# Kernel optimization log

Hardware: AMD Instinct MI355X
Metric: run time of the kernel (lower is better)

Reference implementation:

```python
import jax, jax.numpy as jnp
import numpy as np

N_NODES = 100000
N_EDGES = 1600000
IN_FEATS = 128
OUT_FEATS = 64


def setup_inputs() -> dict:
    key = jax.random.key(0)
    k1, k2, k3, k4 = jax.random.split(key, 4)
    feat = jax.random.normal(k1, (N_NODES, IN_FEATS), dtype=jnp.float32)
    W = jax.random.normal(k2, (IN_FEATS, OUT_FEATS), dtype=jnp.float32) * (1.0 / np.sqrt(IN_FEATS))
    src = jax.random.randint(k3, (N_EDGES,), 0, N_NODES, dtype=jnp.int64)
    dst = jax.random.randint(k4, (N_EDGES,), 0, N_NODES, dtype=jnp.int64)
    return {"feat": feat, "W": W, "src": src, "dst": dst}


def reference(feat, W, src, dst):
    # Linear projection (bias=False): homogeneous graph -> shared fc
    ft = feat @ W  # [N, out]

    # per-edge dot-product score: e_ij = <ft[src], ft[dst]>
    a = jnp.sum(ft[src] * ft[dst], axis=-1)  # [E]

    # edge softmax segmented by destination node (numerically stable)
    neg_inf = jnp.finfo(a.dtype).min
    m = jax.ops.segment_max(a, dst, num_segments=N_NODES)  # [N]
    m = jnp.where(m == neg_inf, 0.0, m)  # guard zero-in-degree nodes
    e = jnp.exp(a - m[dst])  # [E]
    s = jax.ops.segment_sum(e, dst, num_segments=N_NODES)  # [N]
    s = jnp.where(s == 0.0, 1.0, s)
    sa = e / s[dst]  # [E]

    # weighted scatter-sum aggregation: out[i] = sum_{j in N(i)} sa_ij * ft[j]
    rst = jax.ops.segment_sum(ft[src] * sa[:, None], dst, num_segments=N_NODES)
    return rst
```

## Files before the change

### kernel.cpp

```cpp
#include <hip/hip_runtime.h>
#include <hip/hip_fp16.h>
#include <math.h>

#define N_NODES 100000
#define N_EDGES 1600000
#define IN_F    128
#define OUT_F   64
#define K_BKT     196
#define BKT_SHIFT 9
#define BKT_NODES 512
#define BKT_CAP   10240
#define QCAP      3072
#define CHUNK     4096
#define PBLKS     ((N_EDGES + CHUNK - 1) / CHUNK)
#define LTILES    (N_NODES / 16)
#define LBLKS     ((LTILES + 3) / 4)

typedef _Float16 half8 __attribute__((ext_vector_type(8)));
typedef _Float16 h2 __attribute__((ext_vector_type(2)));
typedef _Float16 h4 __attribute__((ext_vector_type(4)));
typedef __fp16   q2v __attribute__((ext_vector_type(2)));
typedef float    f32x4 __attribute__((ext_vector_type(4)));

__device__ __forceinline__ float fdot2f(h2 a, h2 b, float c) {
#if __has_builtin(__builtin_amdgcn_fdot2)
    return __builtin_amdgcn_fdot2(__builtin_bit_cast(q2v, a), __builtin_bit_cast(q2v, b), c, false);
#else
    return (float)a[0] * (float)b[0] + (float)a[1] * (float)b[1] + c;
#endif
}

#if __has_builtin(__builtin_amdgcn_update_dpp)
#define DPP_ADD(x, ctrl)                                                                  \
    (x) += __builtin_bit_cast(float, __builtin_amdgcn_update_dpp(                         \
               0, __builtin_bit_cast(int, (x)), (ctrl), 0xF, 0xF, true))
#define REDUCE16(x) do { DPP_ADD(x, 0xB1); DPP_ADD(x, 0x4E); \
                         DPP_ADD(x, 0x141); DPP_ADD(x, 0x140); } while (0)
#else
#define REDUCE16(x) do { x += __shfl_xor(x, 1); x += __shfl_xor(x, 2); \
                         x += __shfl_xor(x, 4); x += __shfl_xor(x, 8); } while (0)
#endif


__global__ __launch_bounds__(256) void partition_linear_kernel(const int* __restrict__ src,
                                                               const int* __restrict__ dst,
                                                               unsigned* __restrict__ staging,
                                                               int* __restrict__ pcnt,
                                                               int* __restrict__ pbase,
                                                               const float* __restrict__ feat,
                                                               const float* __restrict__ W,
                                                               __half* __restrict__ fth) {
    __shared__ int hist[256], lbase[256], sc[256];
    __shared__ unsigned sval[CHUNK];
    int t = threadIdx.x;
    if (blockIdx.x < PBLKS) {
        hist[t] = 0;
        __syncthreads();
        int beg = blockIdx.x * CHUNK;
        int end = min(beg + CHUNK, N_EDGES);
        for (int i = beg + t; i < end; i += 256)
            atomicAdd(&hist[dst[i] >> BKT_SHIFT], 1);
        __syncthreads();
        int v = hist[t];
        sc[t] = v;
        __syncthreads();
        for (int off = 1; off < 256; off <<= 1) {
            int add = (t >= off) ? sc[t - off] : 0;
            __syncthreads();
            sc[t] += add;
            __syncthreads();
        }
        int lb = sc[t] - v;
        lbase[t] = lb;
        pcnt[blockIdx.x * 256 + t]  = v;
        pbase[blockIdx.x * 256 + t] = lb;
        hist[t] = 0;
        __syncthreads();
        for (int i = beg + t; i < end; i += 256) {
            int s = src[i], d = dst[i];
            int b = d >> BKT_SHIFT;
            int r = atomicAdd(&hist[b], 1);
            sval[lbase[b] + r] = (unsigned)s | ((unsigned)(d & (BKT_NODES - 1)) << 17);
        }
        __syncthreads();
        int n = end - beg;
        for (int p = t; p < n; p += 256)
            staging[(size_t)blockIdx.x * CHUNK + p] = sval[p];
        return;
    }
    int gwave = (blockIdx.x - PBLKS) * 4 + (t >> 6);
    if (gwave >= LTILES) return;
    int lane = t & 63;
    int m = lane & 15, kg = lane >> 4;
    int r0 = gwave * 16;

    half8 fb[4][4];
#pragma unroll
    for (int kb = 0; kb < 4; ++kb)
#pragma unroll
        for (int nb = 0; nb < 4; ++nb) {
            const float* wp = W + (size_t)(kb * 32 + kg * 8) * OUT_F + nb * 16 + m;
#pragma unroll
            for (int j = 0; j < 8; ++j)
                fb[kb][nb][j] = (_Float16)wp[j * OUT_F];
        }

    f32x4 acc[4];
#pragma unroll
    for (int nb = 0; nb < 4; ++nb) acc[nb] = (f32x4){0.f, 0.f, 0.f, 0.f};

#pragma unroll
    for (int kb = 0; kb < 4; ++kb) {
        const float4* ap = (const float4*)(feat + (size_t)(r0 + m) * IN_F + kb * 32 + kg * 8);
        float4 a0 = ap[0], a1 = ap[1];
        half8 fa = {(_Float16)a0.x, (_Float16)a0.y, (_Float16)a0.z, (_Float16)a0.w,
                    (_Float16)a1.x, (_Float16)a1.y, (_Float16)a1.z, (_Float16)a1.w};
#pragma unroll
        for (int nb = 0; nb < 4; ++nb)
            acc[nb] = __builtin_amdgcn_mfma_f32_16x16x32_f16(fa, fb[kb][nb], acc[nb], 0, 0, 0);
    }
#pragma unroll
    for (int nb = 0; nb < 4; ++nb)
#pragma unroll
        for (int i = 0; i < 4; ++i)
            fth[(size_t)(r0 + kg * 4 + i) * OUT_F + nb * 16 + m] = __float2half_rn(acc[nb][i]);
}

__global__ __launch_bounds__(1024) void place_fused_kernel(const unsigned* __restrict__ staging,
                                                           const int* __restrict__ pcnt,
                                                           const int* __restrict__ pbase,
                                                           const __half* __restrict__ fth,
                                                           float* __restrict__ out) {
    const float LOG2E = 1.44269504088896340736f;
    __shared__ unsigned sbuf[BKT_CAP];
    __shared__ int exo[PBLKS], pbs[PBLKS], scnt[PBLKS];
    __shared__ int s512[512];
    __shared__ int cnt[128], rbeg[128], lcur[128];
    __shared__ int csr[QCAP];
    __shared__ int ntot;
    int t = threadIdx.x;
    int b = blockIdx.x >> 2, qb = blockIdx.x & 3;

    int d = 0;
    if (t < PBLKS) { d = pcnt[t * 256 + b]; pbs[t] = pbase[t * 256 + b]; scnt[t] = d; }
    if (t < 512) s512[t] = (t < PBLKS) ? d : 0;
    if (t < 128) cnt[t] = 0;
    __syncthreads();
    for (int off = 1; off < 512; off <<= 1) {
        int add = (t >= off && t < 512) ? s512[t - off] : 0;
        __syncthreads();
        if (t < 512) s512[t] += add;
        __syncthreads();
    }
    if (t < PBLKS) exo[t] = s512[t] - d;
    if (t == PBLKS - 1) ntot = s512[t];
    __syncthreads();
    int n = ntot;

    {
        int wid = t >> 6, ln = t & 63;
        for (int s = wid; s < PBLKS; s += 16) {
            int c = scnt[s], eo = exo[s];
            size_t gb = (size_t)s * CHUNK + pbs[s];
            for (int j = ln; j < c; j += 64)
                sbuf[eo + j] = staging[gb + j];
        }
    }
    __syncthreads();

    for (int i = t; i < n; i += 1024) {
        int nl = sbuf[i] >> 17;
        if ((nl >> 7) == qb) atomicAdd(&cnt[nl & 127], 1);
    }
    __syncthreads();
    if (t < 128) s512[t] = cnt[t];
    __syncthreads();
    for (int off = 1; off < 128; off <<= 1) {
        int add = (t >= off && t < 128) ? s512[t - off] : 0;
        __syncthreads();
        if (t < 128) s512[t] += add;
        __syncthreads();
    }
    if (t < 128) { int v = cnt[t]; int b0 = s512[t] - v; rbeg[t] = b0; lcur[t] = b0; }
    __syncthreads();
    for (int i = t; i < n; i += 1024) {
        unsigned u = sbuf[i];
        int nl = u >> 17;
        if ((nl >> 7) == qb) {
            int pos = atomicAdd(&lcur[nl & 127], 1);
            csr[pos] = (int)(u & 0x1FFFFu);
        }
    }
    __syncthreads();

    int wid = t >> 6, lane = t & 63;
    int q = lane >> 4, ql = lane & 15;
    const _Float16* fh = (const _Float16*)fth;
#pragma unroll
    for (int k = 0; k < 8; ++k) {
        int ln = wid + 16 * k;
        int node = b * BKT_NODES + qb * 128 + ln;
        int beg = rbeg[ln];
        int end = beg + cnt[ln];

        h4 rdv = (node < N_NODES)
                   ? *(const h4*)(fh + (size_t)node * OUT_F + 4 * ql) : (h4){0, 0, 0, 0};
        h2 dlo = __builtin_shufflevector(rdv, rdv, 0, 1);
        h2 dhi = __builtin_shufflevector(rdv, rdv, 2, 3);

        float m = -1e30f, l = 0.f;
        float a0 = 0.f, a1 = 0.f, a2 = 0.f, a3 = 0.f;

        for (int i = beg; i < end; i += 16) {
            int e0 = i + q, e1 = e0 + 4, e2 = e0 + 8, e3 = e0 + 12;
            bool u0 = e0 < end, u1 = e1 < end, u2 = e2 < end, u3 = e3 < end;
            int s0 = csr[u0 ? e0 : beg];
            int s1 = csr[u1 ? e1 : beg];
            int s2 = csr[u2 ? e2 : beg];
            int s3 = csr[u3 ? e3 : beg];
            h4 rA = *(const h4*)(fh + (size_t)s0 * OUT_F + 4 * ql);
            h4 rB = *(const h4*)(fh + (size_t)s1 * OUT_F + 4 * ql);
            h4 rC = *(const h4*)(fh + (size_t)s2 * OUT_F + 4 * ql);
            h4 rD = *(const h4*)(fh + (size_t)s3 * OUT_F + 4 * ql);

            float p0 = fdot2f(__builtin_shufflevector(rA, rA, 0, 1), dlo,
                       fdot2f(__builtin_shufflevector(rA, rA, 2, 3), dhi, 0.f));
            float p1 = fdot2f(__builtin_shufflevector(rB, rB, 0, 1), dlo,
                       fdot2f(__builtin_shufflevector(rB, rB, 2, 3), dhi, 0.f));
            float p2 = fdot2f(__builtin_shufflevector(rC, rC, 0, 1), dlo,
                       fdot2f(__builtin_shufflevector(rC, rC, 2, 3), dhi, 0.f));
            float p3 = fdot2f(__builtin_shufflevector(rD, rD, 0, 1), dlo,
                       fdot2f(__builtin_shufflevector(rD, rD, 2, 3), dhi, 0.f));
            REDUCE16(p0);
            REDUCE16(p1);
            REDUCE16(p2);
            REDUCE16(p3);
            p0 = u0 ? p0 * LOG2E : -1e30f;
            p1 = u1 ? p1 * LOG2E : -1e30f;
            p2 = u2 ? p2 * LOG2E : -1e30f;
            p3 = u3 ? p3 * LOG2E : -1e30f;

            float nm = fmaxf(fmaxf(fmaxf(p0, p1), fmaxf(p2, p3)), m);
            float alpha = exp2f(m - nm);
            float w0 = exp2f(p0 - nm), w1 = exp2f(p1 - nm);
            float w2 = exp2f(p2 - nm), w3 = exp2f(p3 - nm);
            l = l * alpha + ((w0 + w1) + (w2 + w3));
#if __has_builtin(__builtin_amdgcn_cvt_pkrtz)
            h2 wlo = __builtin_bit_cast(h2, __builtin_amdgcn_cvt_pkrtz(w0, w1));
            h2 whi = __builtin_bit_cast(h2, __builtin_amdgcn_cvt_pkrtz(w2, w3));
#else
            h2 wlo = {(_Float16)w0, (_Float16)w1};
            h2 whi = {(_Float16)w2, (_Float16)w3};
#endif
            h2 cab0 = {rA[0], rB[0]}, ccd0 = {rC[0], rD[0]};
            h2 cab1 = {rA[1], rB[1]}, ccd1 = {rC[1], rD[1]};
            h2 cab2 = {rA[2], rB[2]}, ccd2 = {rC[2], rD[2]};
            h2 cab3 = {rA[3], rB[3]}, ccd3 = {rC[3], rD[3]};
            a0 = fdot2f(wlo, cab0, fdot2f(whi, ccd0, a0 * alpha));
            a1 = fdot2f(wlo, cab1, fdot2f(whi, ccd1, a1 * alpha));
            a2 = fdot2f(wlo, cab2, fdot2f(whi, ccd2, a2 * alpha));
            a3 = fdot2f(wlo, cab3, fdot2f(whi, ccd3, a3 * alpha));
            m = nm;
        }

#pragma unroll
        for (int dd = 16; dd <= 32; dd <<= 1) {
            float m2 = __shfl_xor(m, dd), l2 = __shfl_xor(l, dd);
            float b0 = __shfl_xor(a0, dd), b1 = __shfl_xor(a1, dd);
            float b2 = __shfl_xor(a2, dd), b3 = __shfl_xor(a3, dd);
            float M = fmaxf(m, m2);
            float e1 = exp2f(m - M), e2 = exp2f(m2 - M);
            l = l * e1 + l2 * e2;
            a0 = a0 * e1 + b0 * e2;
            a1 = a1 * e1 + b1 * e2;
            a2 = a2 * e1 + b2 * e2;
            a3 = a3 * e1 + b3 * e2;
            m = M;
        }
        if (q == 0 && node < N_NODES) {
            float inv = (l > 0.f) ? 1.f / l : 0.f;
            *(float4*)(out + (size_t)node * OUT_F + 4 * ql) =
                make_float4(a0 * inv, a1 * inv, a2 * inv, a3 * inv);
        }
    }
}

extern "C" void kernel_launch(void* const* d_in, const int* in_sizes, int n_in,
                              void* d_out, int out_size, void* d_ws, size_t ws_size,
                              hipStream_t stream) {
    const float* feat = (const float*)d_in[0];
    const float* W    = (const float*)d_in[1];
    const int*   src  = (const int*)d_in[2];
    const int*   dst  = (const int*)d_in[3];
    float* out = (float*)d_out;

    __half*   fth      = (__half*)d_ws;
    unsigned* staging  = (unsigned*)((int*)d_ws + (size_t)N_NODES * OUT_F / 2);
    int*      pcnt     = (int*)(staging + (size_t)PBLKS * CHUNK);
    int*      pbase    = pcnt + PBLKS * 256;

    partition_linear_kernel<<<PBLKS + LBLKS, 256, 0, stream>>>(src, dst, staging, pcnt, pbase,
                                                               feat, W, fth);
    place_fused_kernel<<<K_BKT * 4, 1024, 0, stream>>>(staging, pcnt, pbase, fth, out);
}
```

Measured before the change: 208.0 us.

## Partition edges into 128-node buckets so each block loads only its own edges

The partition kernel now builds a 1024-bin histogram keyed by 128-node quarter-buckets instead of 256 bins of 512 nodes. Each fused block therefore reads only the edges of its own 128 destination nodes, where previously four blocks each reloaded a full 512-node bucket and filtered it. The staging copy also changes so each wave serves 8 segments at once with 8 lanes per segment. In exchange, the pcnt/pbase tables are four times larger and the per-segment copies are shorter and less coalesced.

```diff
diff --git a/kernel.cpp b/kernel.cpp
--- a/kernel.cpp
+++ b/kernel.cpp
@@ -6,10 +6,9 @@
 #define N_EDGES 1600000
 #define IN_F    128
 #define OUT_F   64
-#define K_BKT     196
-#define BKT_SHIFT 9
-#define BKT_NODES 512
-#define BKT_CAP   10240
+#define NQ        782
+#define Q_SHIFT   7
+#define Q_NODES   128
 #define QCAP      3072
 #define CHUNK     4096
 #define PBLKS     ((N_EDGES + CHUNK - 1) / CHUNK)
@@ -50,19 +49,20 @@
                                                                const float* __restrict__ feat,
                                                                const float* __restrict__ W,
                                                                __half* __restrict__ fth) {
-    __shared__ int hist[256], lbase[256], sc[256];
+    __shared__ int hist[1024], lbase[1024], sc[256];
     __shared__ unsigned sval[CHUNK];
     int t = threadIdx.x;
     if (blockIdx.x < PBLKS) {
-        hist[t] = 0;
+        hist[t] = 0; hist[t + 256] = 0; hist[t + 512] = 0; hist[t + 768] = 0;
         __syncthreads();
         int beg = blockIdx.x * CHUNK;
         int end = min(beg + CHUNK, N_EDGES);
         for (int i = beg + t; i < end; i += 256)
-            atomicAdd(&hist[dst[i] >> BKT_SHIFT], 1);
-        __syncthreads();
-        int v = hist[t];
-        sc[t] = v;
+            atomicAdd(&hist[dst[i] >> Q_SHIFT], 1);
+        __syncthreads();
+        int h0 = hist[4 * t], h1 = hist[4 * t + 1], h2i = hist[4 * t + 2], h3 = hist[4 * t + 3];
+        int tot = h0 + h1 + h2i + h3;
+        sc[t] = tot;
         __syncthreads();
         for (int off = 1; off < 256; off <<= 1) {
             int add = (t >= off) ? sc[t - off] : 0;
@@ -70,17 +70,18 @@
             sc[t] += add;
             __syncthreads();
         }
-        int lb = sc[t] - v;
-        lbase[t] = lb;
-        pcnt[blockIdx.x * 256 + t]  = v;
-        pbase[blockIdx.x * 256 + t] = lb;
-        hist[t] = 0;
+        int excl = sc[t] - tot;
+        int b0 = excl, b1 = excl + h0, b2 = b1 + h1, b3 = b2 + h2i;
+        lbase[4 * t] = b0; lbase[4 * t + 1] = b1; lbase[4 * t + 2] = b2; lbase[4 * t + 3] = b3;
+        *(int4*)(pcnt  + (size_t)blockIdx.x * 1024 + 4 * t) = make_int4(h0, h1, h2i, h3);
+        *(int4*)(pbase + (size_t)blockIdx.x * 1024 + 4 * t) = make_int4(b0, b1, b2, b3);
+        hist[4 * t] = 0; hist[4 * t + 1] = 0; hist[4 * t + 2] = 0; hist[4 * t + 3] = 0;
         __syncthreads();
         for (int i = beg + t; i < end; i += 256) {
             int s = src[i], d = dst[i];
-            int b = d >> BKT_SHIFT;
+            int b = d >> Q_SHIFT;
             int r = atomicAdd(&hist[b], 1);
-            sval[lbase[b] + r] = (unsigned)s | ((unsigned)(d & (BKT_NODES - 1)) << 17);
+            sval[lbase[b] + r] = (unsigned)s | ((unsigned)(d & (Q_NODES - 1)) << 17);
         }
         __syncthreads();
         int n = end - beg;
@@ -126,25 +127,25 @@
             fth[(size_t)(r0 + kg * 4 + i) * OUT_F + nb * 16 + m] = __float2half_rn(acc[nb][i]);
 }
 
-__global__ __launch_bounds__(1024) void place_fused_kernel(const unsigned* __restrict__ staging,
-                                                           const int* __restrict__ pcnt,
-                                                           const int* __restrict__ pbase,
-                                                           const __half* __restrict__ fth,
-                                                           float* __restrict__ out) {
+__global__ __launch_bounds__(1024) void quarter_fused_kernel(const unsigned* __restrict__ staging,
+                                                             const int* __restrict__ pcnt,
+                                                             const int* __restrict__ pbase,
+                                                             const __half* __restrict__ fth,
+                                                             float* __restrict__ out) {
     const float LOG2E = 1.44269504088896340736f;
-    __shared__ unsigned sbuf[BKT_CAP];
+    __shared__ unsigned sbuf[QCAP];
+    __shared__ int csr[QCAP];
     __shared__ int exo[PBLKS], pbs[PBLKS], scnt[PBLKS];
     __shared__ int s512[512];
-    __shared__ int cnt[128], rbeg[128], lcur[128];
-    __shared__ int csr[QCAP];
+    __shared__ int cnt[Q_NODES], rbeg[Q_NODES], lcur[Q_NODES];
     __shared__ int ntot;
     int t = threadIdx.x;
-    int b = blockIdx.x >> 2, qb = blockIdx.x & 3;
+    int qq = blockIdx.x;
 
     int d = 0;
-    if (t < PBLKS) { d = pcnt[t * 256 + b]; pbs[t] = pbase[t * 256 + b]; scnt[t] = d; }
+    if (t < PBLKS) { d = pcnt[(size_t)t * 1024 + qq]; pbs[t] = pbase[(size_t)t * 1024 + qq]; scnt[t] = d; }
     if (t < 512) s512[t] = (t < PBLKS) ? d : 0;
-    if (t < 128) cnt[t] = 0;
+    if (t < Q_NODES) cnt[t] = 0;
     __syncthreads();
     for (int off = 1; off < 512; off <<= 1) {
         int add = (t >= off && t < 512) ? s512[t - off] : 0;
@@ -159,37 +160,33 @@
 
     {
         int wid = t >> 6, ln = t & 63;
-        for (int s = wid; s < PBLKS; s += 16) {
+        int sg0 = wid * 8 + (ln >> 3), j0 = ln & 7;
+        for (int s = sg0; s < PBLKS; s += 128) {
             int c = scnt[s], eo = exo[s];
             size_t gb = (size_t)s * CHUNK + pbs[s];
-            for (int j = ln; j < c; j += 64)
+            for (int j = j0; j < c; j += 8)
                 sbuf[eo + j] = staging[gb + j];
         }
     }
     __syncthreads();
 
-    for (int i = t; i < n; i += 1024) {
-        int nl = sbuf[i] >> 17;
-        if ((nl >> 7) == qb) atomicAdd(&cnt[nl & 127], 1);
-    }
-    __syncthreads();
-    if (t < 128) s512[t] = cnt[t];
-    __syncthreads();
-    for (int off = 1; off < 128; off <<= 1) {
-        int add = (t >= off && t < 128) ? s512[t - off] : 0;
-        __syncthreads();
-        if (t < 128) s512[t] += add;
-        __syncthreads();
-    }
-    if (t < 128) { int v = cnt[t]; int b0 = s512[t] - v; rbeg[t] = b0; lcur[t] = b0; }
+    for (int i = t; i < n; i += 1024)
+        atomicAdd(&cnt[sbuf[i] >> 17], 1);
+    __syncthreads();
+    if (t < Q_NODES) s512[t] = cnt[t];
+    __syncthreads();
+    for (int off = 1; off < Q_NODES; off <<= 1) {
+        int add = (t >= off && t < Q_NODES) ? s512[t - off] : 0;
+        __syncthreads();
+        if (t < Q_NODES) s512[t] += add;
+        __syncthreads();
+    }
+    if (t < Q_NODES) { int v = cnt[t]; int b0 = s512[t] - v; rbeg[t] = b0; lcur[t] = b0; }
     __syncthreads();
     for (int i = t; i < n; i += 1024) {
         unsigned u = sbuf[i];
-        int nl = u >> 17;
-        if ((nl >> 7) == qb) {
-            int pos = atomicAdd(&lcur[nl & 127], 1);
-            csr[pos] = (int)(u & 0x1FFFFu);
-        }
+        int pos = atomicAdd(&lcur[u >> 17], 1);
+        csr[pos] = (int)(u & 0x1FFFFu);
     }
     __syncthreads();
 
@@ -199,7 +196,7 @@
 #pragma unroll
     for (int k = 0; k < 8; ++k) {
         int ln = wid + 16 * k;
-        int node = b * BKT_NODES + qb * 128 + ln;
+        int node = qq * Q_NODES + ln;
         int beg = rbeg[ln];
         int end = beg + cnt[ln];
 
@@ -297,9 +294,9 @@
     __half*   fth      = (__half*)d_ws;
     unsigned* staging  = (unsigned*)((int*)d_ws + (size_t)N_NODES * OUT_F / 2);
     int*      pcnt     = (int*)(staging + (size_t)PBLKS * CHUNK);
-    int*      pbase    = pcnt + PBLKS * 256;
+    int*      pbase    = pcnt + (size_t)PBLKS * 1024;
 
     partition_linear_kernel<<<PBLKS + LBLKS, 256, 0, stream>>>(src, dst, staging, pcnt, pbase,
                                                                feat, W, fth);
-    place_fused_kernel<<<K_BKT * 4, 1024, 0, stream>>>(staging, pcnt, pbase, fth, out);
+    quarter_fused_kernel<<<NQ, 1024, 0, stream>>>(staging, pcnt, pbase, fth, out);
 }
```

Result: faster. 188.4 us (-9.4%).
